# Performance work log

Measured on AMD Instinct MI355X. Metric: run time of the kernel, lower is better.

Reference implementation:

```python
import jax, jax.numpy as jnp
import numpy as np

N = 100000
D = 64
E = 1600000
EPS = 1e-5


def setup_inputs() -> dict:
    key = jax.random.key(0)
    k1, k2, k3, k4, k5, k6 = jax.random.split(key, 6)
    node_features = jax.random.normal(k1, (N, D), dtype=jnp.float32)
    edge_index = jax.random.randint(k2, (E, 2), 0, N, dtype=jnp.int64)
    # torch Linear params: W [out, in], b [out]
    lim_m = 1.0 / np.sqrt(2 * D)
    W_msg = jax.random.uniform(k3, (D, 2 * D), minval=-lim_m, maxval=lim_m, dtype=jnp.float32)
    b_msg = jax.random.uniform(k4, (D,), minval=-lim_m, maxval=lim_m, dtype=jnp.float32)
    W_upd = jax.random.uniform(k5, (D, 2 * D), minval=-lim_m, maxval=lim_m, dtype=jnp.float32)
    b_upd = jax.random.uniform(k6, (D,), minval=-lim_m, maxval=lim_m, dtype=jnp.float32)
    gamma = jnp.ones((D,), dtype=jnp.float32)
    beta = jnp.zeros((D,), dtype=jnp.float32)
    return {
        "node_features": node_features,
        "edge_index": edge_index,
        "W_msg": W_msg,
        "b_msg": b_msg,
        "W_upd": W_upd,
        "b_upd": b_upd,
        "gamma": gamma,
        "beta": beta,
    }


def _layer_norm(x, gamma, beta):
    mu = jnp.mean(x, axis=-1, keepdims=True)
    var = jnp.mean(jnp.square(x - mu), axis=-1, keepdims=True)
    return (x - mu) * jax.lax.rsqrt(var + EPS) * gamma + beta


def reference(node_features, edge_index, W_msg, b_msg, W_upd, b_upd, gamma, beta):
    src = edge_index[:, 0]
    tgt = edge_index[:, 1]
    # per-edge message: relu(Linear(cat(x[src], x[tgt])))  -- split weight to avoid [E,2D] concat
    Wm_s = W_msg[:, :D]  # [D, D] applied to src feats
    Wm_t = W_msg[:, D:]  # [D, D] applied to tgt feats
    msg = jax.nn.relu(node_features[src] @ Wm_s.T + node_features[tgt] @ Wm_t.T + b_msg)  # [E, D]
    # scatter-mean into target nodes
    messages = jax.ops.segment_sum(msg, tgt, num_segments=N)  # [N, D]
    counts = jax.ops.segment_sum(jnp.ones((edge_index.shape[0],), dtype=node_features.dtype), tgt, num_segments=N)
    counts = jnp.maximum(counts, 1.0)[:, None]
    messages = messages / counts
    # update: relu(Linear(cat(x, messages))) + residual + LayerNorm
    Wu_x = W_upd[:, :D]
    Wu_m = W_upd[:, D:]
    updated = jax.nn.relu(node_features @ Wu_x.T + messages @ Wu_m.T + b_upd)
    return _layer_norm(updated + node_features, gamma, beta)
```

## Files before the change

### kernel.cpp

```cpp
#include <hip/hip_runtime.h>
#include <hip/hip_bf16.h>
#include <stdint.h>

#define NNODES 100000
#define DF 64
#define NEDGES 1600000
#define ND (NNODES * DF)
#define BKT 100
#define NBUCK 1000
#define CHUNK 128
#define NCHUNK (NEDGES / CHUNK)
#define NPW 25

static __device__ __forceinline__ float bf2f(unsigned short u) {
    union { uint32_t i; float f; } c; c.i = ((uint32_t)u) << 16; return c.f;
}
static __device__ __forceinline__ unsigned short f2bf(float f) {
    union { __hip_bfloat16 b; unsigned short u; } c; c.b = __float2bfloat16(f); return c.u;
}
static __device__ __forceinline__ void unpack2(uint32_t u, float& lo, float& hi) {
    union { uint32_t i; float f; } a, b;
    a.i = u << 16; b.i = u & 0xFFFF0000u;
    lo = a.f; hi = b.f;
}

__global__ void wconv_k(const unsigned short* __restrict__ x,
                        const unsigned int* __restrict__ eiu,
                        const void* __restrict__ Wm, const void* __restrict__ Wu,
                        const void* __restrict__ bm, const void* __restrict__ bu,
                        const void* __restrict__ ga, const void* __restrict__ be,
                        float* __restrict__ WfMT, float* __restrict__ WfUT,
                        float* __restrict__ prm, int* __restrict__ flags) {
    __shared__ int cnt_sane, cnt_odd_nz;
    if (threadIdx.x == 0) { cnt_sane = 0; cnt_odd_nz = 0; }
    __syncthreads();
    {
        unsigned short s = x[threadIdx.x * 2];
        unsigned short m = s & 0x7FFF;
        if (m < 0x0080 || (m >= 0x3000 && m <= 0x4200)) atomicAdd(&cnt_sane, 1);
        if (threadIdx.x < 64) {
            if (eiu[threadIdx.x * 2 + 1] != 0u) atomicAdd(&cnt_odd_nz, 1);
        }
    }
    __syncthreads();
    const int bf = (cnt_sane >= 192) ? 1 : 0;
    if (blockIdx.x == 0 && threadIdx.x == 0) {
        flags[0] = bf;
        flags[1] = (cnt_odd_nz == 0) ? 1 : 0;
    }
    int i = blockIdx.x * 256 + threadIdx.x;
    if (i < 16384) {
        const void* src = (i < 8192) ? Wm : Wu;
        float* dst = (i < 8192) ? WfMT : WfUT;
        int ii = i & 8191, j = ii >> 6, k = ii & 63;
        int si = (j & 63) * 128 + ((j >> 6) ? 64 : 0) + k;
        float v = bf ? bf2f(((const unsigned short*)src)[si]) : ((const float*)src)[si];
        dst[(j >> 6) * 4096 + k * 64 + (j & 63)] = v;
    } else if (i < 16384 + 320) {
        int t = i - 16384, which = t >> 6, k = t & 63;
        if (which == 4) { prm[t] = 0.f; }
        else {
            const void* p = (which == 0) ? bm : (which == 1) ? bu : (which == 2) ? ga : be;
            prm[t] = bf ? bf2f(((const unsigned short*)p)[k]) : ((const float*)p)[k];
        }
    }
}

__global__ __launch_bounds__(256, 1) void pj_k(const int* __restrict__ flags,
                                               const void* __restrict__ xv,
                                               const float* __restrict__ WfMT,
                                               const float* __restrict__ prm,
                                               unsigned short* __restrict__ Ps,
                                               unsigned short* __restrict__ Pt,
                                               const int* __restrict__ ei,
                                               int* __restrict__ BktCnt) {
    const int blk = blockIdx.x;
    if (blk < 2048) {
        const int lane = threadIdx.x & 63;
        const int wib = __builtin_amdgcn_readfirstlane(threadIdx.x >> 6);
        const int bf = flags[0];
        const int mtx = (blk >= 1024);
        const float* WT = WfMT + (mtx ? 4096 : 0);

        float w[64];
        #pragma unroll
        for (int k = 0; k < 64; ++k) w[k] = WT[k * 64 + lane];
        const float bs = mtx ? prm[lane] : 0.f;
        unsigned short* outp = mtx ? Pt : Ps;

        const int wv = (blk & 1023) * 4 + wib;
        const int n0 = wv * NPW;
        if (n0 >= NNODES) return;
        const int n1 = (n0 + NPW < NNODES) ? n0 + NPW : NNODES;
        for (int n = n0; n < n1; ++n) {
            float a0 = 0.f, a1 = 0.f, a2 = 0.f, a3 = 0.f;
            if (bf) {
                const uint4* xr = (const uint4*)((const unsigned short*)xv + (size_t)n * DF);
                #pragma unroll
                for (int q = 0; q < 8; ++q) {
                    uint4 v = xr[q];
                    float x0,x1,x2,x3,x4,x5,x6,x7;
                    unpack2(v.x, x0, x1); unpack2(v.y, x2, x3);
                    unpack2(v.z, x4, x5); unpack2(v.w, x6, x7);
                    a0 = fmaf(x0, w[8*q+0], a0); a1 = fmaf(x1, w[8*q+1], a1);
                    a2 = fmaf(x2, w[8*q+2], a2); a3 = fmaf(x3, w[8*q+3], a3);
                    a0 = fmaf(x4, w[8*q+4], a0); a1 = fmaf(x5, w[8*q+5], a1);
                    a2 = fmaf(x6, w[8*q+6], a2); a3 = fmaf(x7, w[8*q+7], a3);
                }
            } else {
                const float4* xr = (const float4*)((const float*)xv + (size_t)n * DF);
                #pragma unroll
                for (int q = 0; q < 16; ++q) {
                    float4 v = xr[q];
                    a0 = fmaf(v.x, w[4*q+0], a0); a1 = fmaf(v.y, w[4*q+1], a1);
                    a2 = fmaf(v.z, w[4*q+2], a2); a3 = fmaf(v.w, w[4*q+3], a3);
                }
            }
            outp[(size_t)n * DF + lane] = f2bf((a0 + a1) + (a2 + a3) + bs);
        }
    } else {
        __shared__ int h[NBUCK];
        const int i64 = flags[1];
        const int hb = blk - 2048;
        for (int i = threadIdx.x; i < NBUCK; i += 256) h[i] = 0;
        __syncthreads();
        for (int e = hb * 256 + threadIdx.x; e < NEDGES; e += 65536) {
            int tgt = i64 ? ei[4*e + 2] : ei[2*e + 1];
            if ((unsigned)tgt < NNODES) atomicAdd(&h[tgt / BKT], 1);
        }
        __syncthreads();
        for (int b = threadIdx.x; b < NBUCK; b += 256)
            if (h[b]) atomicAdd(BktCnt + b, h[b]);
    }
}

__global__ __launch_bounds__(1024) void bscan_k(const int* __restrict__ BktCnt,
                                                int* __restrict__ BktOff,
                                                int* __restrict__ BktCur) {
    __shared__ int lds[1024];
    int t = threadIdx.x;
    int c = (t < NBUCK) ? BktCnt[t] : 0;
    lds[t] = c;
    __syncthreads();
    for (int off = 1; off < 1024; off <<= 1) {
        int add = (t >= off) ? lds[t - off] : 0;
        __syncthreads();
        lds[t] += add;
        __syncthreads();
    }
    if (t < NBUCK) {
        int ex = lds[t] - c;
        BktOff[t] = ex;
        BktCur[t] = ex;
    }
    if (t == NBUCK - 1) BktOff[NBUCK] = lds[t];
}

__global__ __launch_bounds__(256) void bfill_k(const int* __restrict__ flags,
                                               const int* __restrict__ ei,
                                               int* __restrict__ BktCur,
                                               int* __restrict__ BktE) {
    __shared__ int h[NBUCK], h2[NBUCK], basee[NBUCK];
    const int i64 = flags[1];
    for (int i = threadIdx.x; i < NBUCK; i += 256) { h[i] = 0; h2[i] = 0; }
    __syncthreads();
    const int stride = gridDim.x * 256;
    for (int e = blockIdx.x * 256 + threadIdx.x; e < NEDGES; e += stride) {
        int tgt = i64 ? ei[4*e + 2] : ei[2*e + 1];
        if ((unsigned)tgt < NNODES) atomicAdd(&h[tgt / BKT], 1);
    }
    __syncthreads();
    for (int b = threadIdx.x; b < NBUCK; b += 256)
        if (h[b]) basee[b] = atomicAdd(BktCur + b, h[b]);
    __syncthreads();
    for (int e = blockIdx.x * 256 + threadIdx.x; e < NEDGES; e += stride) {
        int src, tgt;
        if (i64) { src = ei[4*e]; tgt = ei[4*e + 2]; }
        else     { src = ei[2*e]; tgt = ei[2*e + 1]; }
        if ((unsigned)tgt >= NNODES) continue;
        int b = tgt / BKT;
        int tl = tgt - b * BKT;
        int r = atomicAdd(&h2[b], 1);
        BktE[basee[b] + r] = (tl << 24) | (src & 0xFFFFFF);
    }
}

__global__ __launch_bounds__(256) void tsort_k(const int* __restrict__ BktOff,
                                               const int* __restrict__ BktE,
                                               int* __restrict__ CsrSrc,
                                               int* __restrict__ Row) {
    __shared__ int oc[128], excl[128], cur[128];
    const int tid = threadIdx.x;
    const int b = blockIdx.x;
    const int s = BktOff[b], e = BktOff[b + 1];
    const int n = e - s;
    if (tid < 128) { oc[tid] = 0; }
    __syncthreads();
    for (int i = tid; i < n; i += 256)
        atomicAdd(&oc[((unsigned)BktE[s + i]) >> 24], 1);
    __syncthreads();
    if (tid < 128) excl[tid] = (tid > 0) ? oc[tid - 1] : 0;
    __syncthreads();
    for (int off = 1; off < 128; off <<= 1) {
        int add = (tid >= off && tid < 128) ? excl[tid - off] : 0;
        __syncthreads();
        if (tid < 128) excl[tid] += add;
        __syncthreads();
    }
    if (tid < BKT) {
        Row[b * BKT + tid] = s + excl[tid];
        cur[tid] = excl[tid];
    }
    if (b == 0 && tid == 0) Row[NNODES] = NEDGES;
    __syncthreads();
    for (int i = tid; i < n; i += 256) {
        int v = BktE[s + i];
        int tl = ((unsigned)v) >> 24;
        int p = atomicAdd(&cur[tl], 1);
        int sv = v & 0xFFFFFF;
        if (sv >= NNODES) sv = 0;
        CsrSrc[s + p] = sv << 6;
    }
}

__global__ __launch_bounds__(256) void cstart_k(const int* __restrict__ Row,
                                                int* __restrict__ ChunkT) {
    int c = blockIdx.x * 256 + threadIdx.x;
    if (c > NCHUNK) return;
    if (c == NCHUNK) { ChunkT[NCHUNK] = NNODES; return; }
    int target = c * CHUNK;
    int lo = 0, hi = NNODES + 1;
    while (lo < hi) { int mid = (lo + hi) >> 1; if (Row[mid] >= target) hi = mid; else lo = mid + 1; }
    ChunkT[c] = lo;
}

__global__ __launch_bounds__(256) void agg_k(const unsigned short* __restrict__ Ps,
                                             const unsigned short* __restrict__ Pt,
                                             const int* __restrict__ Row,
                                             const int* __restrict__ CsrSrc,
                                             const int* __restrict__ ChunkT,
                                             unsigned short* __restrict__ Msg) {
    const int lane = threadIdx.x & 63;
    const int wib = __builtin_amdgcn_readfirstlane(threadIdx.x >> 6);
    const int w = blockIdx.x * 4 + wib;
    if (w >= NCHUNK) return;

    const int t_lo = ChunkT[w];
    const int t_hi = ChunkT[w + 1];
    if (t_lo >= t_hi) return;

    int segS = Row[t_lo];
    for (int t = t_lo; t < t_hi; ++t) {
        const int segE = Row[t + 1];
        const int deg = segE - segS;
        float ptv = bf2f(Pt[(size_t)t * DF + lane]);
        float pa0 = 0.f, pa1 = 0.f, pa2 = 0.f, pa3 = 0.f;
        for (int i = segS; i < segE; i += 16) {
            #pragma unroll
            for (int j = 0; j < 16; ++j) {
                const int idx = i + j;
                const int ok = idx < segE;
                const int sv = CsrSrc[ok ? idx : segS];
                float p = bf2f(Ps[(size_t)(unsigned)sv + lane]);
                float v = ok ? fmaxf(p + ptv, 0.f) : 0.f;
                if ((j & 3) == 0)      pa0 += v;
                else if ((j & 3) == 1) pa1 += v;
                else if ((j & 3) == 2) pa2 += v;
                else                   pa3 += v;
            }
        }
        float macc = (pa0 + pa1) + (pa2 + pa3);
        float mval = (deg > 0) ? (macc / (float)deg) : 0.f;
        Msg[(size_t)t * DF + lane] = f2bf(mval);
        segS = segE;
    }
}

__global__ __launch_bounds__(256, 1) void mm_k(const int* __restrict__ flags,
                                               const void* __restrict__ xv,
                                               const float* __restrict__ WT,
                                               const float* __restrict__ bias,
                                               void* __restrict__ outv,
                                               int of) {
    const int lane = threadIdx.x & 63;
    const int wib = __builtin_amdgcn_readfirstlane(threadIdx.x >> 6);
    const int bf = flags[0];

    float w[64];
    #pragma unroll
    for (int k = 0; k < 64; ++k) w[k] = WT[k * 64 + lane];
    const float bs = bias[lane];

    const int wv = blockIdx.x * 4 + wib;
    const int n0 = wv * NPW;
    if (n0 >= NNODES) return;
    const int n1 = (n0 + NPW < NNODES) ? n0 + NPW : NNODES;
    for (int n = n0; n < n1; ++n) {
        float a0 = 0.f, a1 = 0.f, a2 = 0.f, a3 = 0.f;
        if (bf) {
            const uint4* xr = (const uint4*)((const unsigned short*)xv + (size_t)n * DF);
            #pragma unroll
            for (int q = 0; q < 8; ++q) {
                uint4 v = xr[q];
                float x0,x1,x2,x3,x4,x5,x6,x7;
                unpack2(v.x, x0, x1); unpack2(v.y, x2, x3);
                unpack2(v.z, x4, x5); unpack2(v.w, x6, x7);
                a0 = fmaf(x0, w[8*q+0], a0); a1 = fmaf(x1, w[8*q+1], a1);
                a2 = fmaf(x2, w[8*q+2], a2); a3 = fmaf(x3, w[8*q+3], a3);
                a0 = fmaf(x4, w[8*q+4], a0); a1 = fmaf(x5, w[8*q+5], a1);
                a2 = fmaf(x6, w[8*q+6], a2); a3 = fmaf(x7, w[8*q+7], a3);
            }
        } else {
            const float4* xr = (const float4*)((const float*)xv + (size_t)n * DF);
            #pragma unroll
            for (int q = 0; q < 16; ++q) {
                float4 v = xr[q];
                a0 = fmaf(v.x, w[4*q+0], a0); a1 = fmaf(v.y, w[4*q+1], a1);
                a2 = fmaf(v.z, w[4*q+2], a2); a3 = fmaf(v.w, w[4*q+3], a3);
            }
        }
        float r = (a0 + a1) + (a2 + a3) + bs;
        size_t gi = (size_t)n * DF + lane;
        if (of) ((float*)outv)[gi] = r;
        else    ((unsigned short*)outv)[gi] = f2bf(r);
    }
}

__global__ __launch_bounds__(256, 1) void u2_k(const int* __restrict__ flags,
                                               const void* __restrict__ xv,
                                               const unsigned short* __restrict__ Msg,
                                               const float* __restrict__ t1,
                                               const float* __restrict__ WT,
                                               const float* __restrict__ prm,
                                               void* __restrict__ outv) {
    const int lane = threadIdx.x & 63;
    const int wib = __builtin_amdgcn_readfirstlane(threadIdx.x >> 6);
    const int bf = flags[0];

    float w[64];
    #pragma unroll
    for (int k = 0; k < 64; ++k) w[k] = WT[k * 64 + lane];
    const float ga = prm[128 + lane];
    const float be = prm[192 + lane];

    const unsigned short* x16 = (const unsigned short*)xv;
    const float* xf = (const float*)xv;

    const int wv = blockIdx.x * 4 + wib;
    const int n0 = wv * NPW;
    if (n0 >= NNODES) return;
    const int n1 = (n0 + NPW < NNODES) ? n0 + NPW : NNODES;
    for (int n = n0; n < n1; ++n) {
        float b0 = 0.f, b1 = 0.f, b2 = 0.f, b3 = 0.f;
        const uint4* mw = (const uint4*)(Msg + (size_t)n * DF);
        #pragma unroll
        for (int q = 0; q < 8; ++q) {
            uint4 v = mw[q];
            float m0,m1,m2,m3,m4,m5,m6,m7;
            unpack2(v.x, m0, m1); unpack2(v.y, m2, m3);
            unpack2(v.z, m4, m5); unpack2(v.w, m6, m7);
            b0 = fmaf(m0, w[8*q+0], b0); b1 = fmaf(m1, w[8*q+1], b1);
            b2 = fmaf(m2, w[8*q+2], b2); b3 = fmaf(m3, w[8*q+3], b3);
            b0 = fmaf(m4, w[8*q+4], b0); b1 = fmaf(m5, w[8*q+5], b1);
            b2 = fmaf(m6, w[8*q+6], b2); b3 = fmaf(m7, w[8*q+7], b3);
        }
        size_t gi = (size_t)n * DF + lane;
        float t  = t1[gi];
        float xl = bf ? bf2f(x16[gi]) : xf[gi];
        float u = fmaxf((b0 + b1) + (b2 + b3) + t, 0.f);
        float r = u + xl;

        float s = r, s2 = r * r;
        #pragma unroll
        for (int m = 1; m < 64; m <<= 1) {
            s  += __shfl_xor(s, m, 64);
            s2 += __shfl_xor(s2, m, 64);
        }
        float mu  = s * (1.0f / 64.0f);
        float var = fmaxf(s2 * (1.0f / 64.0f) - mu * mu, 0.f);
        float o = (r - mu) * rsqrtf(var + 1e-5f) * ga + be;

        if (bf) ((__hip_bfloat16*)outv)[gi] = __float2bfloat16(o);
        else    ((float*)outv)[gi] = o;
    }
}

extern "C" void kernel_launch(void* const* d_in, const int* in_sizes, int n_in,
                              void* d_out, int out_size, void* d_ws, size_t ws_size,
                              hipStream_t stream) {
    const void* x  = d_in[0];
    const int*  ei = (const int*)d_in[1];
    const void* Wm = d_in[2];
    const void* bm = d_in[3];
    const void* Wu = d_in[4];
    const void* bu = d_in[5];
    const void* ga = d_in[6];
    const void* be = d_in[7];

    char* ws = (char*)d_ws;
    size_t off = 0;
    unsigned short* Ps  = (unsigned short*)(ws + off); off += (size_t)ND * 2;
    unsigned short* Pt  = (unsigned short*)(ws + off); off += (size_t)ND * 2;
    unsigned short* Msg = (unsigned short*)(ws + off); off += (size_t)ND * 2;
    int*   BktE   = (int*)(ws + off); off += (size_t)NEDGES * 4;
    int*   CsrSrc = (int*)(ws + off); off += (size_t)NEDGES * 4;
    int*   Row    = (int*)(ws + off); off += (size_t)(NNODES + 1) * 4;
    int*   BktCnt = (int*)(ws + off); off += NBUCK * 4;
    int*   BktOff = (int*)(ws + off); off += (NBUCK + 1) * 4;
    int*   BktCur = (int*)(ws + off); off += NBUCK * 4;
    int*   flg    = (int*)(ws + off); off += 16;
    float* WfMT   = (float*)(ws + off); off += 8192 * 4;
    float* WfUT   = (float*)(ws + off); off += 8192 * 4;
    float* prm    = (float*)(ws + off); off += 320 * 4;

    float* t1 = (float*)Ps;
    int* ChunkT = BktE;

    (void)hipMemsetAsync(BktCnt, 0, NBUCK * 4, stream);

    wconv_k<<<66, 256, 0, stream>>>((const unsigned short*)x, (const unsigned int*)ei,
                                    Wm, Wu, bm, bu, ga, be, WfMT, WfUT, prm, flg);

    pj_k<<<2304, 256, 0, stream>>>(flg, x, WfMT, prm, Ps, Pt, ei, BktCnt);

    bscan_k<<<1, 1024, 0, stream>>>(BktCnt, BktOff, BktCur);
    bfill_k<<<128, 256, 0, stream>>>(flg, ei, BktCur, BktE);
    tsort_k<<<NBUCK, 256, 0, stream>>>(BktOff, BktE, CsrSrc, Row);

    cstart_k<<<(NCHUNK + 256) / 256, 256, 0, stream>>>(Row, ChunkT);

    agg_k<<<(NCHUNK + 3) / 4, 256, 0, stream>>>(Ps, Pt, Row, CsrSrc, ChunkT, Msg);

    mm_k<<<1024, 256, 0, stream>>>(flg, x, WfUT, prm + 64, t1, 1);

    u2_k<<<1024, 256, 0, stream>>>(flg, x, Msg, t1, WfUT + 4096, prm, d_out);
}
```

Measured before the change: 321.7 us.

## Reuse per-block bucket histograms in fill, fold memset and chunk search into kernels

The histogram blocks in the projection kernel now save their per-block bucket counts (256 blocks, up from the earlier hardcoded stride) into a scratch buffer. The fill kernel reuses these counts instead of rereading edge targets to rebuild its own histogram, which removes one full pass over the edge list. The BktCnt memset moves into the weight-conversion kernel, and the separate chunk-start binary-search kernel is dropped: agg_k now runs the binary searches inline per wave. This cuts two launches and redundant edge reads, at the cost of a larger scratch buffer that aliases CsrSrc and of repeated binary searches in agg_k.

```diff
diff --git a/kernel.cpp b/kernel.cpp
--- a/kernel.cpp
+++ b/kernel.cpp
@@ -11,6 +11,7 @@
 #define CHUNK 128
 #define NCHUNK (NEDGES / CHUNK)
 #define NPW 25
+#define NHB 256
 
 static __device__ __forceinline__ float bf2f(unsigned short u) {
     union { uint32_t i; float f; } c; c.i = ((uint32_t)u) << 16; return c.f;
@@ -30,7 +31,8 @@
                         const void* __restrict__ bm, const void* __restrict__ bu,
                         const void* __restrict__ ga, const void* __restrict__ be,
                         float* __restrict__ WfMT, float* __restrict__ WfUT,
-                        float* __restrict__ prm, int* __restrict__ flags) {
+                        float* __restrict__ prm, int* __restrict__ flags,
+                        int* __restrict__ BktCnt) {
     __shared__ int cnt_sane, cnt_odd_nz;
     if (threadIdx.x == 0) { cnt_sane = 0; cnt_odd_nz = 0; }
     __syncthreads();
@@ -49,6 +51,7 @@
         flags[1] = (cnt_odd_nz == 0) ? 1 : 0;
     }
     int i = blockIdx.x * 256 + threadIdx.x;
+    if (i < NBUCK) BktCnt[i] = 0;
     if (i < 16384) {
         const void* src = (i < 8192) ? Wm : Wu;
         float* dst = (i < 8192) ? WfMT : WfUT;
@@ -73,7 +76,8 @@
                                                unsigned short* __restrict__ Ps,
                                                unsigned short* __restrict__ Pt,
                                                const int* __restrict__ ei,
-                                               int* __restrict__ BktCnt) {
+                                               int* __restrict__ BktCnt,
+                                               int* __restrict__ HBlk) {
     const int blk = blockIdx.x;
     if (blk < 2048) {
         const int lane = threadIdx.x & 63;
@@ -124,13 +128,16 @@
         const int hb = blk - 2048;
         for (int i = threadIdx.x; i < NBUCK; i += 256) h[i] = 0;
         __syncthreads();
-        for (int e = hb * 256 + threadIdx.x; e < NEDGES; e += 65536) {
+        for (int e = hb * 256 + threadIdx.x; e < NEDGES; e += NHB * 256) {
             int tgt = i64 ? ei[4*e + 2] : ei[2*e + 1];
             if ((unsigned)tgt < NNODES) atomicAdd(&h[tgt / BKT], 1);
         }
         __syncthreads();
-        for (int b = threadIdx.x; b < NBUCK; b += 256)
-            if (h[b]) atomicAdd(BktCnt + b, h[b]);
+        for (int b = threadIdx.x; b < NBUCK; b += 256) {
+            int v = h[b];
+            HBlk[hb * NBUCK + b] = v;
+            if (v) atomicAdd(BktCnt + b, v);
+        }
     }
 }
 
@@ -158,22 +165,20 @@
 
 __global__ __launch_bounds__(256) void bfill_k(const int* __restrict__ flags,
                                                const int* __restrict__ ei,
+                                               const int* __restrict__ HBlk,
                                                int* __restrict__ BktCur,
                                                int* __restrict__ BktE) {
-    __shared__ int h[NBUCK], h2[NBUCK], basee[NBUCK];
+    __shared__ int h2[NBUCK], basee[NBUCK];
     const int i64 = flags[1];
-    for (int i = threadIdx.x; i < NBUCK; i += 256) { h[i] = 0; h2[i] = 0; }
-    __syncthreads();
-    const int stride = gridDim.x * 256;
-    for (int e = blockIdx.x * 256 + threadIdx.x; e < NEDGES; e += stride) {
-        int tgt = i64 ? ei[4*e + 2] : ei[2*e + 1];
-        if ((unsigned)tgt < NNODES) atomicAdd(&h[tgt / BKT], 1);
-    }
-    __syncthreads();
-    for (int b = threadIdx.x; b < NBUCK; b += 256)
-        if (h[b]) basee[b] = atomicAdd(BktCur + b, h[b]);
-    __syncthreads();
-    for (int e = blockIdx.x * 256 + threadIdx.x; e < NEDGES; e += stride) {
+    const int blk = blockIdx.x;
+    for (int i = threadIdx.x; i < NBUCK; i += 256) h2[i] = 0;
+    __syncthreads();
+    for (int b = threadIdx.x; b < NBUCK; b += 256) {
+        int hv = HBlk[blk * NBUCK + b];
+        basee[b] = hv ? atomicAdd(BktCur + b, hv) : 0;
+    }
+    __syncthreads();
+    for (int e = blk * 256 + threadIdx.x; e < NEDGES; e += NHB * 256) {
         int src, tgt;
         if (i64) { src = ei[4*e]; tgt = ei[4*e + 2]; }
         else     { src = ei[2*e]; tgt = ei[2*e + 1]; }
@@ -223,30 +228,28 @@
     }
 }
 
-__global__ __launch_bounds__(256) void cstart_k(const int* __restrict__ Row,
-                                                int* __restrict__ ChunkT) {
-    int c = blockIdx.x * 256 + threadIdx.x;
-    if (c > NCHUNK) return;
-    if (c == NCHUNK) { ChunkT[NCHUNK] = NNODES; return; }
-    int target = c * CHUNK;
-    int lo = 0, hi = NNODES + 1;
-    while (lo < hi) { int mid = (lo + hi) >> 1; if (Row[mid] >= target) hi = mid; else lo = mid + 1; }
-    ChunkT[c] = lo;
-}
-
 __global__ __launch_bounds__(256) void agg_k(const unsigned short* __restrict__ Ps,
                                              const unsigned short* __restrict__ Pt,
                                              const int* __restrict__ Row,
                                              const int* __restrict__ CsrSrc,
-                                             const int* __restrict__ ChunkT,
                                              unsigned short* __restrict__ Msg) {
     const int lane = threadIdx.x & 63;
     const int wib = __builtin_amdgcn_readfirstlane(threadIdx.x >> 6);
     const int w = blockIdx.x * 4 + wib;
     if (w >= NCHUNK) return;
 
-    const int t_lo = ChunkT[w];
-    const int t_hi = ChunkT[w + 1];
+    const int eA = w * CHUNK;
+    int lo = 0, hi = NNODES + 1;
+    while (lo < hi) { int mid = (lo + hi) >> 1; if (Row[mid] >= eA) hi = mid; else lo = mid + 1; }
+    const int t_lo = lo;
+    int t_hi;
+    if (w == NCHUNK - 1) t_hi = NNODES;
+    else {
+        const int hiB = eA + CHUNK;
+        lo = t_lo; hi = NNODES + 1;
+        while (lo < hi) { int mid = (lo + hi) >> 1; if (Row[mid] >= hiB) hi = mid; else lo = mid + 1; }
+        t_hi = (lo > NNODES) ? NNODES : lo;
+    }
     if (t_lo >= t_hi) return;
 
     int segS = Row[t_lo];
@@ -414,22 +417,20 @@
     float* prm    = (float*)(ws + off); off += 320 * 4;
 
     float* t1 = (float*)Ps;
-    int* ChunkT = BktE;
-
-    (void)hipMemsetAsync(BktCnt, 0, NBUCK * 4, stream);
+    int* HBlk = CsrSrc;
 
     wconv_k<<<66, 256, 0, stream>>>((const unsigned short*)x, (const unsigned int*)ei,
-                                    Wm, Wu, bm, bu, ga, be, WfMT, WfUT, prm, flg);
-
-    pj_k<<<2304, 256, 0, stream>>>(flg, x, WfMT, prm, Ps, Pt, ei, BktCnt);
+                                    Wm, Wu, bm, bu, ga, be, WfMT, WfUT, prm, flg, BktCnt);
+
+    pj_k<<<2048 + NHB, 256, 0, stream>>>(flg, x, WfMT, prm, Ps, Pt, ei, BktCnt, HBlk);
 
     bscan_k<<<1, 1024, 0, stream>>>(BktCnt, BktOff, BktCur);
-    bfill_k<<<128, 256, 0, stream>>>(flg, ei, BktCur, BktE);
+
+    bfill_k<<<NHB, 256, 0, stream>>>(flg, ei, HBlk, BktCur, BktE);
+
     tsort_k<<<NBUCK, 256, 0, stream>>>(BktOff, BktE, CsrSrc, Row);
 
-    cstart_k<<<(NCHUNK + 256) / 256, 256, 0, stream>>>(Row, ChunkT);
-
-    agg_k<<<(NCHUNK + 3) / 4, 256, 0, stream>>>(Ps, Pt, Row, CsrSrc, ChunkT, Msg);
+    agg_k<<<(NCHUNK + 3) / 4, 256, 0, stream>>>(Ps, Pt, Row, CsrSrc, Msg);
 
     mm_k<<<1024, 256, 0, stream>>>(flg, x, WfUT, prm + 64, t1, 1);
 
```

Result: faster. 302.2 us (-6.0%).
